# Kernel optimization log

Measured on AMD Instinct MI355X. Metric: run time of the kernel, lower is better.

The kernel has to match this reference:

```python
import jax, jax.numpy as jnp
import numpy as np

S, D, H = 4096, 2048, 16
HD = D // H

def setup_inputs() -> dict:
    key = jax.random.key(0)
    ks = jax.random.split(key, 9)
    s = 1.0 / np.sqrt(D)
    return {
        "hidden_states": jax.random.normal(ks[0], (S, D), jnp.float32),
        "Wq": jax.random.uniform(ks[1], (D, D), jnp.float32, -s, s),
        "bq": jax.random.uniform(ks[2], (D,), jnp.float32, -s, s),
        "Wk": jax.random.uniform(ks[3], (D, D), jnp.float32, -s, s),
        "bk": jax.random.uniform(ks[4], (D,), jnp.float32, -s, s),
        "Wv": jax.random.uniform(ks[5], (D, D), jnp.float32, -s, s),
        "bv": jax.random.uniform(ks[6], (D,), jnp.float32, -s, s),
        "Wo": jax.random.uniform(ks[7], (D, D), jnp.float32, -s, s),
        "bo": jax.random.uniform(ks[8], (D,), jnp.float32, -s, s),
    }

def reference(hidden_states, Wq, bq, Wk, bk, Wv, bv, Wo, bo):
    seq = hidden_states.shape[0]
    # projections (torch Linear: x @ W.T + b)
    q = (hidden_states @ Wq.T + bq).reshape(seq, H, HD).transpose(1, 0, 2)  # [H,S,hd]
    k = (hidden_states @ Wk.T + bk).reshape(seq, H, HD).transpose(1, 0, 2)
    v = (hidden_states @ Wv.T + bv).reshape(seq, H, HD).transpose(1, 0, 2)
    scale = 1.0 / np.sqrt(HD).astype(np.float32)
    qk = jnp.einsum('hqd,hkd->hqk', q, k) * scale  # [H,S,S]
    causal = jnp.tril(jnp.ones((seq, seq), bool))
    qk = jnp.where(causal, qk, -jnp.inf)
    attn = jax.nn.softmax(qk, axis=-1)
    out = jnp.einsum('hqk,hkd->hqd', attn, v)  # [H,S,hd]
    out = out.transpose(1, 0, 2).reshape(seq, D)
    return out @ Wo.T + bo
```

## Files before the change

### kernel.cpp

```cpp
#include <hip/hip_runtime.h>
#include <stdint.h>

#define S_LEN 4096
#define D_DIM 2048
#define NHEAD 16
#define HDIM  128

typedef short bf16x8 __attribute__((ext_vector_type(8)));
typedef float f32x4  __attribute__((ext_vector_type(4)));
typedef float f32x16 __attribute__((ext_vector_type(16)));

__device__ __forceinline__ unsigned short f2bf(float x) {
  union { float f; unsigned u; } v; v.f = x;
  unsigned r = v.u + 0x7FFFu + ((v.u >> 16) & 1u);
  return (unsigned short)(r >> 16);
}

__device__ __forceinline__ float bf2f(unsigned short s) {
  union { unsigned u; float f; } v; v.u = ((unsigned)s) << 16;
  return v.f;
}

__device__ __forceinline__ unsigned cvtpk_bf16(float lo, float hi_) {
  unsigned r;
  asm("v_cvt_pk_bf16_f32 %0, %1, %2" : "=v"(r) : "v"(lo), "v"(hi_));
  return r;
}

__device__ __forceinline__ void gload_lds16(const void* g, void* l) {
  __builtin_amdgcn_global_load_lds(
      (const __attribute__((address_space(1))) unsigned int*)g,
      (__attribute__((address_space(3))) unsigned int*)l, 16, 0, 0);
}

__global__ __launch_bounds__(256) void cvt_all(
    const float* __restrict__ X, const float* __restrict__ Wq,
    const float* __restrict__ Wk, const float* __restrict__ Wv,
    const float* __restrict__ Wo, unsigned short* __restrict__ out) {
  const size_t DD = (size_t)D_DIM * D_DIM;
  size_t i = ((size_t)blockIdx.x * 256 + threadIdx.x) * 8;
  const float* src; size_t off;
  if (i < 2 * DD)      { src = X;  off = i; }
  else if (i < 3 * DD) { src = Wq; off = i - 2 * DD; }
  else if (i < 4 * DD) { src = Wk; off = i - 3 * DD; }
  else if (i < 5 * DD) { src = Wv; off = i - 4 * DD; }
  else                 { src = Wo; off = i - 5 * DD; }
  float4 a = *(const float4*)(src + off);
  float4 b = *(const float4*)(src + off + 4);
  union { unsigned short s[8]; bf16x8 v; } o;
  o.s[0] = f2bf(a.x); o.s[1] = f2bf(a.y); o.s[2] = f2bf(a.z); o.s[3] = f2bf(a.w);
  o.s[4] = f2bf(b.x); o.s[5] = f2bf(b.y); o.s[6] = f2bf(b.z); o.s[7] = f2bf(b.w);
  *(bf16x8*)(out + i) = o.v;
}

__global__ __launch_bounds__(256, 2) void gemm_qkv(
    const unsigned short* __restrict__ A, const unsigned short* __restrict__ W,
    const float* __restrict__ bq, const float* __restrict__ bk,
    const float* __restrict__ bv, unsigned short* __restrict__ Q,
    unsigned short* __restrict__ Ko, unsigned short* __restrict__ V,
    float qsc) {
  __shared__ __attribute__((aligned(16))) unsigned short As[128 * 32];
  __shared__ __attribute__((aligned(16))) unsigned short Bs[128 * 32];
  const int m0 = blockIdx.y * 128, n0 = blockIdx.x * 128;
  const int tid = threadIdx.x, lane = tid & 63, wv = tid >> 6;
  const int wm = wv >> 1, wn = wv & 1;
  const int rA = lane & 15, kb = (lane >> 4) * 8;
  const int K = D_DIM;

  f32x4 acc[4][4];
#pragma unroll
  for (int i = 0; i < 4; ++i)
#pragma unroll
    for (int j = 0; j < 4; ++j)
#pragma unroll
      for (int r = 0; r < 4; ++r) acc[i][j][r] = 0.f;

  for (int k0 = 0; k0 < K; k0 += 32) {
    __syncthreads();
#pragma unroll
    for (int p = 0; p < 2; ++p) {
      const int rr = (wv * 2 + p) * 16 + (lane >> 2);
      const int cc = lane & 3;
      gload_lds16(A + (size_t)(m0 + rr) * K + k0 + cc * 8, As + (wv * 2 + p) * 512);
      gload_lds16(W + (size_t)(n0 + rr) * K + k0 + cc * 8, Bs + (wv * 2 + p) * 512);
    }
    __syncthreads();
    bf16x8 af[4], bfr[4];
#pragma unroll
    for (int i = 0; i < 4; ++i)
      af[i] = *(const bf16x8*)(As + (wm * 64 + i * 16 + rA) * 32 + kb);
#pragma unroll
    for (int j = 0; j < 4; ++j)
      bfr[j] = *(const bf16x8*)(Bs + (wn * 64 + j * 16 + rA) * 32 + kb);
#pragma unroll
    for (int i = 0; i < 4; ++i)
#pragma unroll
      for (int j = 0; j < 4; ++j)
        acc[i][j] = __builtin_amdgcn_mfma_f32_16x16x32_bf16(af[i], bfr[j], acc[i][j], 0, 0, 0);
  }

  const int cR = (lane >> 4) * 4, cC = lane & 15;
#pragma unroll
  for (int j = 0; j < 4; ++j) {
    const int col = n0 + wn * 64 + j * 16 + cC;
    const int seg = col >> 11, cl = col & 2047;
    const float* bp = (seg == 0) ? bq : (seg == 1) ? bk : bv;
    unsigned short* op = (seg == 0) ? Q : (seg == 1) ? Ko : V;
    const float es = (seg == 0) ? qsc : 1.0f;
    const float bvv = bp[cl];
#pragma unroll
    for (int i = 0; i < 4; ++i) {
      const int row0 = m0 + wm * 64 + i * 16 + cR;
#pragma unroll
      for (int r = 0; r < 4; ++r)
        op[(size_t)(row0 + r) * D_DIM + cl] = f2bf((acc[i][j][r] + bvv) * es);
    }
  }
}

__global__ __launch_bounds__(256, 2) void gemm_bt_f32(
    const unsigned short* __restrict__ A, const unsigned short* __restrict__ B,
    const float* __restrict__ bias, float* __restrict__ Cout,
    int M, int N, int K) {
  __shared__ __attribute__((aligned(16))) unsigned short As[128 * 32];
  __shared__ __attribute__((aligned(16))) unsigned short Bs[128 * 32];
  const int m0 = blockIdx.y * 128, n0 = blockIdx.x * 128;
  const int tid = threadIdx.x, lane = tid & 63, wv = tid >> 6;
  const int wm = wv >> 1, wn = wv & 1;
  const int rA = lane & 15, kb = (lane >> 4) * 8;

  f32x4 acc[4][4];
#pragma unroll
  for (int i = 0; i < 4; ++i)
#pragma unroll
    for (int j = 0; j < 4; ++j)
#pragma unroll
      for (int r = 0; r < 4; ++r) acc[i][j][r] = 0.f;

  for (int k0 = 0; k0 < K; k0 += 32) {
    __syncthreads();
#pragma unroll
    for (int p = 0; p < 2; ++p) {
      const int rr = (wv * 2 + p) * 16 + (lane >> 2);
      const int cc = lane & 3;
      gload_lds16(A + (size_t)(m0 + rr) * K + k0 + cc * 8, As + (wv * 2 + p) * 512);
      gload_lds16(B + (size_t)(n0 + rr) * K + k0 + cc * 8, Bs + (wv * 2 + p) * 512);
    }
    __syncthreads();
    bf16x8 af[4], bfr[4];
#pragma unroll
    for (int i = 0; i < 4; ++i)
      af[i] = *(const bf16x8*)(As + (wm * 64 + i * 16 + rA) * 32 + kb);
#pragma unroll
    for (int j = 0; j < 4; ++j)
      bfr[j] = *(const bf16x8*)(Bs + (wn * 64 + j * 16 + rA) * 32 + kb);
#pragma unroll
    for (int i = 0; i < 4; ++i)
#pragma unroll
      for (int j = 0; j < 4; ++j)
        acc[i][j] = __builtin_amdgcn_mfma_f32_16x16x32_bf16(af[i], bfr[j], acc[i][j], 0, 0, 0);
  }

  const int cR = (lane >> 4) * 4, cC = lane & 15;
#pragma unroll
  for (int j = 0; j < 4; ++j) {
    const int col = n0 + wn * 64 + j * 16 + cC;
    const float bvv = bias[col];
#pragma unroll
    for (int i = 0; i < 4; ++i) {
      const int row0 = m0 + wm * 64 + i * 16 + cR;
#pragma unroll
      for (int r = 0; r < 4; ++r)
        Cout[(size_t)(row0 + r) * N + col] = acc[i][j][r] + bvv;
    }
  }
}

__global__ __launch_bounds__(256, 2) void attn_part(
    const unsigned short* __restrict__ Qb, const unsigned short* __restrict__ Kb,
    const unsigned short* __restrict__ Vb, unsigned short* __restrict__ Opart,
    float* __restrict__ ML) {
  __shared__ __attribute__((aligned(16))) unsigned short Ks[64 * 128];
  __shared__ __attribute__((aligned(16))) unsigned short Vt[128 * 64];
  const int bid = blockIdx.x;
  const int h  = ((bid & 7) << 1) | ((bid >> 3) & 1);
  const int hf = (bid >> 4) & 1;
  const int qi = 31 - (bid >> 5);
  const int q0 = qi * 128;
  const int u2 = (h * 32 + qi) * 2 + hf;
  const int tid = threadIdx.x, lane = tid & 63, wv = tid >> 6;
  const int qc = lane & 31, hi = lane >> 5;
  const int q0w = q0 + wv * 32;
  const int myq = q0w + qc;
  const int kp = tid & 31, hb = (tid >> 5) * 16;

  bf16x8 qf[8];
#pragma unroll
  for (int sl = 0; sl < 8; ++sl)
    qf[sl] = *(const bf16x8*)(Qb + (size_t)myq * D_DIM + h * HDIM + sl * 16 + hi * 8);

  f32x16 oacc[4];
#pragma unroll
  for (int nf = 0; nf < 4; ++nf)
#pragma unroll
    for (int r = 0; r < 16; ++r) oacc[nf][r] = 0.f;
  float mh = -3.0e38f, l = 0.f;

  const int klo = hf * (qi + 1), khi = klo + qi + 1;
  const int wqmax = q0w + 31;

  for (int kt = klo; kt < khi; ++kt) {
    const int k0 = kt * 64;
    __syncthreads();
#pragma unroll
    for (int p = 0; p < 4; ++p) {
      const int ob = wv * 4096 + p * 1024;
      const int o = ob + lane * 16;
      const int r = o >> 8, c = (o >> 4) & 15;
      gload_lds16(Kb + (size_t)(k0 + r) * D_DIM + h * HDIM + (c ^ (r & 7)) * 8,
                  Ks + ob / 2);
    }
    {
      const unsigned short* s0 = Vb + (size_t)(k0 + 2 * kp) * D_DIM + h * HDIM + hb;
      union { uint4 u[4]; unsigned short s[32]; } t;
      t.u[0] = *(const uint4*)s0;           t.u[1] = *(const uint4*)(s0 + 8);
      t.u[2] = *(const uint4*)(s0 + D_DIM); t.u[3] = *(const uint4*)(s0 + D_DIM + 8);
#pragma unroll
      for (int w = 0; w < 16; ++w) {
        const int hd = hb + w;
        const unsigned val = (unsigned)t.s[w] | ((unsigned)t.s[16 + w] << 16);
        *(unsigned*)((char*)Vt + hd * 128 + (((kp >> 2) ^ (hd & 7)) << 4) + ((kp & 3) << 2)) = val;
      }
    }
    __syncthreads();
    if (k0 > wqmax) continue;

    f32x16 sacc[2];
#pragma unroll
    for (int kb = 0; kb < 2; ++kb)
#pragma unroll
      for (int r = 0; r < 16; ++r) sacc[kb][r] = 0.f;
    __builtin_amdgcn_s_setprio(1);
#pragma unroll
    for (int sl = 0; sl < 8; ++sl) {
#pragma unroll
      for (int kb = 0; kb < 2; ++kb) {
        const int row = kb * 32 + qc;
        bf16x8 kfr = *(const bf16x8*)((const char*)Ks + row * 256 +
                                      (((2 * sl + hi) ^ (qc & 7)) << 4));
        sacc[kb] = __builtin_amdgcn_mfma_f32_32x32x16_bf16(kfr, qf[sl], sacc[kb], 0, 0, 0);
      }
    }
    __builtin_amdgcn_s_setprio(0);

    const bool needmask = (k0 + 63 > q0w);
    if (needmask) {
      const int dq = myq - k0;
#pragma unroll
      for (int kb = 0; kb < 2; ++kb)
#pragma unroll
        for (int r = 0; r < 16; ++r) {
          const int kk = kb * 32 + (r & 3) + 8 * (r >> 2) + 4 * hi;
          if (kk > dq) sacc[kb][r] = -3.0e38f;
        }
    }
    float mx0[8];
#pragma unroll
    for (int t = 0; t < 8; ++t)
      mx0[t] = fmaxf(fmaxf(sacc[0][t], sacc[0][t + 8]),
                     fmaxf(sacc[1][t], sacc[1][t + 8]));
    float mx = fmaxf(fmaxf(fmaxf(mx0[0], mx0[1]), fmaxf(mx0[2], mx0[3])),
                     fmaxf(fmaxf(mx0[4], mx0[5]), fmaxf(mx0[6], mx0[7])));
    mx = fmaxf(mx, __shfl_xor(mx, 32));
    if (!__all(mx <= mh + 11.5f)) {
      const float mnew = fmaxf(mh, mx);
      const float corr = exp2f(mh - mnew);
      mh = mnew;
      l *= corr;
#pragma unroll
      for (int r = 0; r < 16; ++r) {
        const float cr = __shfl(corr, (r & 3) + 8 * (r >> 2) + 4 * hi);
#pragma unroll
        for (int nf = 0; nf < 4; ++nf) oacc[nf][r] *= cr;
      }
    }
    float rs = 0.f;
#pragma unroll
    for (int kb = 0; kb < 2; ++kb)
#pragma unroll
      for (int r = 0; r < 16; ++r) {
        const float p = exp2f(sacc[kb][r] - mh);
        sacc[kb][r] = p;
        rs += p;
      }
    rs += __shfl_xor(rs, 32);
    l += rs;

    bf16x8 pa[4];
#pragma unroll
    for (int kb = 0; kb < 2; ++kb)
#pragma unroll
      for (int s = 0; s < 2; ++s) {
        const int b = s * 8;
        unsigned pk0 = cvtpk_bf16(sacc[kb][b + 0], sacc[kb][b + 1]);
        unsigned pk1 = cvtpk_bf16(sacc[kb][b + 2], sacc[kb][b + 3]);
        unsigned pk2 = cvtpk_bf16(sacc[kb][b + 4], sacc[kb][b + 5]);
        unsigned pk3 = cvtpk_bf16(sacc[kb][b + 6], sacc[kb][b + 7]);
        const unsigned sw0 = (unsigned)__shfl_xor((int)pk0, 32);
        const unsigned sw1 = (unsigned)__shfl_xor((int)pk1, 32);
        const unsigned sw2 = (unsigned)__shfl_xor((int)pk2, 32);
        const unsigned sw3 = (unsigned)__shfl_xor((int)pk3, 32);
        union { unsigned u[4]; bf16x8 v; } f;
        if (hi) { f.u[0] = sw2; f.u[1] = sw3; f.u[2] = pk2; f.u[3] = pk3; }
        else    { f.u[0] = pk0; f.u[1] = pk1; f.u[2] = sw0; f.u[3] = sw1; }
        pa[kb * 2 + s] = f.v;
      }

    __builtin_amdgcn_s_setprio(1);
#pragma unroll
    for (int nf = 0; nf < 4; ++nf) {
      const int hd = 32 * nf + qc;
#pragma unroll
      for (int ks = 0; ks < 4; ++ks) {
        bf16x8 vf = *(const bf16x8*)((const char*)Vt + hd * 128 +
                                     (((2 * ks + hi) ^ (qc & 7)) << 4));
        oacc[nf] = __builtin_amdgcn_mfma_f32_32x32x16_bf16(pa[ks], vf, oacc[nf], 0, 0, 0);
      }
    }
    __builtin_amdgcn_s_setprio(0);
  }

  unsigned short* ob = Opart + (size_t)u2 * 16384;
#pragma unroll
  for (int r = 0; r < 16; ++r) {
    const int rl = wv * 32 + (r & 3) + 8 * (r >> 2) + 4 * hi;
#pragma unroll
    for (int nf = 0; nf < 4; ++nf)
      ob[rl * 128 + 32 * nf + qc] = f2bf(oacc[nf][r]);
  }
  if (hi == 0) {
    ML[(size_t)u2 * 256 + wv * 32 + qc] = mh;
    ML[(size_t)u2 * 256 + 128 + wv * 32 + qc] = l;
  }
}

__global__ __launch_bounds__(256) void attn_combine(
    const unsigned short* __restrict__ Opart, const float* __restrict__ ML,
    unsigned short* __restrict__ Ob) {
  const int u = blockIdx.x;
  const int h = u >> 5, qi = u & 31;
  const int tid = threadIdx.x;
  const int row = tid >> 1, c0 = (tid & 1) * 64;
  const float m1 = ML[(size_t)(u * 2 + 0) * 256 + row];
  const float l1 = ML[(size_t)(u * 2 + 0) * 256 + 128 + row];
  const float m2 = ML[(size_t)(u * 2 + 1) * 256 + row];
  const float l2 = ML[(size_t)(u * 2 + 1) * 256 + 128 + row];
  const float M  = fmaxf(m1, m2);
  const float a1 = exp2f(m1 - M), a2 = exp2f(m2 - M);
  const float inv = 1.f / (a1 * l1 + a2 * l2);
  const unsigned short* p1 = Opart + (size_t)(u * 2 + 0) * 16384 + row * 128 + c0;
  const unsigned short* p2 = Opart + (size_t)(u * 2 + 1) * 16384 + row * 128 + c0;
  unsigned short* o = Ob + (size_t)(qi * 128 + row) * D_DIM + h * HDIM + c0;
#pragma unroll
  for (int c = 0; c < 64; c += 8) {
    bf16x8 v1 = *(const bf16x8*)(p1 + c);
    bf16x8 v2 = *(const bf16x8*)(p2 + c);
    union { unsigned short s[8]; bf16x8 v; } out;
#pragma unroll
    for (int e = 0; e < 8; ++e)
      out.s[e] = f2bf((bf2f((unsigned short)v1[e]) * a1 +
                       bf2f((unsigned short)v2[e]) * a2) * inv);
    *(bf16x8*)(o + c) = out.v;
  }
}

extern "C" void kernel_launch(void* const* d_in, const int* in_sizes, int n_in,
                              void* d_out, int out_size, void* d_ws, size_t ws_size,
                              hipStream_t stream) {
  const float* X  = (const float*)d_in[0];
  const float* Wq = (const float*)d_in[1];
  const float* bq = (const float*)d_in[2];
  const float* Wk = (const float*)d_in[3];
  const float* bk = (const float*)d_in[4];
  const float* Wv = (const float*)d_in[5];
  const float* bv = (const float*)d_in[6];
  const float* Wo = (const float*)d_in[7];
  const float* bo = (const float*)d_in[8];
  float* out = (float*)d_out;

  unsigned short* ws = (unsigned short*)d_ws;
  const size_t SD = (size_t)S_LEN * D_DIM;
  const size_t DD = (size_t)D_DIM * D_DIM;
  unsigned short* Xb  = ws;
  unsigned short* Wqb = Xb + SD;
  unsigned short* Wob = Wqb + 3 * DD;
  unsigned short* Qb  = Wob + DD;
  unsigned short* Kb  = Qb + SD;
  unsigned short* Vb  = Kb + SD;
  unsigned short* AOb = Vb + SD;
  unsigned short* Opart = ws;
  float* ML = (float*)(ws + SD + 2 * DD);

  cvt_all<<<(int)(6 * DD / 8 / 256), 256, 0, stream>>>(X, Wq, Wk, Wv, Wo, Xb);

  const float qsc = 0.08838834764831845f * 1.4426950408889634f;
  gemm_qkv<<<dim3(48, 32), 256, 0, stream>>>(Xb, Wqb, bq, bk, bv, Qb, Kb, Vb, qsc);

  attn_part<<<dim3(1024), 256, 0, stream>>>(Qb, Kb, Vb, Opart, ML);
  attn_combine<<<dim3(512), 256, 0, stream>>>(Opart, ML, AOb);

  gemm_bt_f32<<<dim3(16, 32), 256, 0, stream>>>(AOb, Wob, bo, out, S_LEN, D_DIM, D_DIM);
}
```

Baseline: 321.8 us.

## Rewrite QKV GEMM with 256x256 tiles, double-buffered swizzled LDS staging

Replaces the 128x128, K=32 QKV projection GEMM with a 512-thread kernel using 256x256 output tiles and K=64 steps. Staging uses double-buffered LDS with an XOR-swizzled layout to avoid bank conflicts. Loads for step t+2 are issued while step t computes, with explicit vmcnt waits and barriers. This aims to raise arithmetic intensity and hide global load latency. In exchange it uses much more LDS and registers per block, and the grid drops to 384 blocks, which may underfill the GPU's compute units.

Result: slower. 336.9 us (+4.7%).

```diff
diff --git a/kernel.cpp b/kernel.cpp
--- a/kernel.cpp
+++ b/kernel.cpp
@@ -53,67 +53,101 @@
   *(bf16x8*)(out + i) = o.v;
 }
 
-__global__ __launch_bounds__(256, 2) void gemm_qkv(
+__device__ __forceinline__ void stage256(
+    const unsigned short* __restrict__ A, const unsigned short* __restrict__ W,
+    unsigned short* la, unsigned short* lb, int m0, int n0, int k0,
+    int wv, int lane) {
+  const int K = 2048;
+#pragma unroll
+  for (int p = 0; p < 4; ++p) {
+    const int off = wv * 1024 + p * 8192;
+    const int o = off + lane * 16;
+    const int half = o >> 14, rowh = (o >> 7) & 127, ch = (o >> 4) & 7;
+    const int row = half * 128 + rowh;
+    const int csrc = (ch ^ (rowh & 7)) * 8;
+    gload_lds16(A + (size_t)(m0 + row) * K + k0 + csrc, la + (off >> 1));
+    gload_lds16(W + (size_t)(n0 + row) * K + k0 + csrc, lb + (off >> 1));
+  }
+}
+
+__global__ __launch_bounds__(512, 1) void gemm_qkv2(
     const unsigned short* __restrict__ A, const unsigned short* __restrict__ W,
     const float* __restrict__ bq, const float* __restrict__ bk,
     const float* __restrict__ bv, unsigned short* __restrict__ Q,
     unsigned short* __restrict__ Ko, unsigned short* __restrict__ V,
     float qsc) {
-  __shared__ __attribute__((aligned(16))) unsigned short As[128 * 32];
-  __shared__ __attribute__((aligned(16))) unsigned short Bs[128 * 32];
-  const int m0 = blockIdx.y * 128, n0 = blockIdx.x * 128;
+  __shared__ __attribute__((aligned(16))) unsigned short LA[2][16384];
+  __shared__ __attribute__((aligned(16))) unsigned short LB[2][16384];
+  const int m0 = blockIdx.y * 256, n0 = blockIdx.x * 256;
   const int tid = threadIdx.x, lane = tid & 63, wv = tid >> 6;
-  const int wm = wv >> 1, wn = wv & 1;
-  const int rA = lane & 15, kb = (lane >> 4) * 8;
-  const int K = D_DIM;
-
-  f32x4 acc[4][4];
-#pragma unroll
-  for (int i = 0; i < 4; ++i)
+  const int wm = wv >> 2, wn = wv & 3;
+  const int rA = lane & 15, g4 = lane >> 4;
+
+  f32x4 acc[8][4];
+#pragma unroll
+  for (int i = 0; i < 8; ++i)
 #pragma unroll
     for (int j = 0; j < 4; ++j)
 #pragma unroll
       for (int r = 0; r < 4; ++r) acc[i][j][r] = 0.f;
 
-  for (int k0 = 0; k0 < K; k0 += 32) {
-    __syncthreads();
-#pragma unroll
-    for (int p = 0; p < 2; ++p) {
-      const int rr = (wv * 2 + p) * 16 + (lane >> 2);
-      const int cc = lane & 3;
-      gload_lds16(A + (size_t)(m0 + rr) * K + k0 + cc * 8, As + (wv * 2 + p) * 512);
-      gload_lds16(W + (size_t)(n0 + rr) * K + k0 + cc * 8, Bs + (wv * 2 + p) * 512);
-    }
-    __syncthreads();
-    bf16x8 af[4], bfr[4];
-#pragma unroll
-    for (int i = 0; i < 4; ++i)
-      af[i] = *(const bf16x8*)(As + (wm * 64 + i * 16 + rA) * 32 + kb);
-#pragma unroll
-    for (int j = 0; j < 4; ++j)
-      bfr[j] = *(const bf16x8*)(Bs + (wn * 64 + j * 16 + rA) * 32 + kb);
-#pragma unroll
-    for (int i = 0; i < 4; ++i)
+  stage256(A, W, &LA[0][0], &LB[0][0], m0, n0, 0, wv, lane);
+  stage256(A, W, &LA[1][0], &LB[1][0], m0, n0, 64, wv, lane);
+  asm volatile("s_waitcnt vmcnt(8)" ::: "memory");
+  __builtin_amdgcn_s_barrier();
+  __builtin_amdgcn_sched_barrier(0);
+
+  for (int t = 0; t < 32; ++t) {
+    const unsigned short* la = &LA[t & 1][0] + wm * 8192;
+    const unsigned short* lb = &LB[t & 1][0] + (wn >> 1) * 8192;
+    const int rbB = (wn & 1) * 64;
+#pragma unroll
+    for (int kk = 0; kk < 2; ++kk) {
+      bf16x8 af[8], bfv[4];
+      const int sw = ((kk * 4 + g4) ^ (rA & 7)) * 8;
+#pragma unroll
+      for (int i = 0; i < 8; ++i)
+        af[i] = *(const bf16x8*)(la + (i * 16 + rA) * 64 + sw);
 #pragma unroll
       for (int j = 0; j < 4; ++j)
-        acc[i][j] = __builtin_amdgcn_mfma_f32_16x16x32_bf16(af[i], bfr[j], acc[i][j], 0, 0, 0);
-  }
-
-  const int cR = (lane >> 4) * 4, cC = lane & 15;
+        bfv[j] = *(const bf16x8*)(lb + (rbB + j * 16 + rA) * 64 + sw);
+      __builtin_amdgcn_s_setprio(1);
+#pragma unroll
+      for (int i = 0; i < 8; ++i)
+#pragma unroll
+        for (int j = 0; j < 4; ++j)
+          acc[i][j] = __builtin_amdgcn_mfma_f32_16x16x32_bf16(af[i], bfv[j], acc[i][j], 0, 0, 0);
+      __builtin_amdgcn_s_setprio(0);
+    }
+    if (t == 31) break;
+    __builtin_amdgcn_s_barrier();
+    __builtin_amdgcn_sched_barrier(0);
+    if (t + 2 < 32) {
+      stage256(A, W, &LA[t & 1][0], &LB[t & 1][0], m0, n0, (t + 2) * 64, wv, lane);
+      asm volatile("s_waitcnt vmcnt(8)" ::: "memory");
+    } else {
+      asm volatile("s_waitcnt vmcnt(0)" ::: "memory");
+    }
+    __builtin_amdgcn_s_barrier();
+    __builtin_amdgcn_sched_barrier(0);
+  }
+
+  const int cR = g4 * 4, cC = rA;
+  const int seg = n0 >> 11;
+  const float* bp = (seg == 0) ? bq : (seg == 1) ? bk : bv;
+  unsigned short* op = (seg == 0) ? Q : (seg == 1) ? Ko : V;
+  const float es = (seg == 0) ? qsc : 1.0f;
+  const int ncl0 = (n0 & 2047) + wn * 64;
 #pragma unroll
   for (int j = 0; j < 4; ++j) {
-    const int col = n0 + wn * 64 + j * 16 + cC;
-    const int seg = col >> 11, cl = col & 2047;
-    const float* bp = (seg == 0) ? bq : (seg == 1) ? bk : bv;
-    unsigned short* op = (seg == 0) ? Q : (seg == 1) ? Ko : V;
-    const float es = (seg == 0) ? qsc : 1.0f;
-    const float bvv = bp[cl];
-#pragma unroll
-    for (int i = 0; i < 4; ++i) {
-      const int row0 = m0 + wm * 64 + i * 16 + cR;
+    const int col = ncl0 + j * 16 + cC;
+    const float bvv = bp[col];
+#pragma unroll
+    for (int i = 0; i < 8; ++i) {
+      const int row0 = m0 + wm * 128 + i * 16 + cR;
 #pragma unroll
       for (int r = 0; r < 4; ++r)
-        op[(size_t)(row0 + r) * D_DIM + cl] = f2bf((acc[i][j][r] + bvv) * es);
+        op[(size_t)(row0 + r) * D_DIM + col] = f2bf((acc[i][j][r] + bvv) * es);
     }
   }
 }
@@ -404,7 +438,7 @@
   cvt_all<<<(int)(6 * DD / 8 / 256), 256, 0, stream>>>(X, Wq, Wk, Wv, Wo, Xb);
 
   const float qsc = 0.08838834764831845f * 1.4426950408889634f;
-  gemm_qkv<<<dim3(48, 32), 256, 0, stream>>>(Xb, Wqb, bq, bk, bv, Qb, Kb, Vb, qsc);
+  gemm_qkv2<<<dim3(24, 16), 512, 0, stream>>>(Xb, Wqb, bq, bk, bv, Qb, Kb, Vb, qsc);
 
   attn_part<<<dim3(1024), 256, 0, stream>>>(Qb, Kb, Vb, Opart, ML);
   attn_combine<<<dim3(512), 256, 0, stream>>>(Opart, ML, AOb);
```
